# Performance work log

Hardware: AMD Instinct MI355X
Metric: run time of the kernel (lower is better)

## Reference

```python
import jax, jax.numpy as jnp
import numpy as np
from functools import partial

H = 512
V = 32000


def setup_inputs() -> dict:
    key = jax.random.key(0)
    ks = jax.random.split(key, 16)
    B, Td, Te = 16, 64, 64
    s = 0.02
    inp = {
        'input_seqs': jax.random.normal(ks[0], (B, Td, H), jnp.float32),
        'input_lengths': jax.random.randint(ks[1], (B,), 1, Td + 1, jnp.int32),
        'encoder_outputs': jax.random.normal(ks[2], (B, Te, H), jnp.float32),
        'encoder_length': jax.random.randint(ks[3], (B,), 1, Te + 1, jnp.int32),
        # GRU (1 layer, batch_first): PyTorch layout W_ih (3H,H), W_hh (3H,H)
        'W_ih': jax.random.normal(ks[4], (3 * H, H), jnp.float32) * s,
        'W_hh': jax.random.normal(ks[5], (3 * H, H), jnp.float32) * s,
        'b_ih': jnp.zeros((3 * H,), jnp.float32),
        'b_hh': jnp.zeros((3 * H,), jnp.float32),
        # Attn: W: Linear(2H -> H), v: Linear(H -> 1)
        'W_attn': jax.random.normal(ks[6], (H, 2 * H), jnp.float32) * s,
        'b_attn': jnp.zeros((H,), jnp.float32),
        'v_w': jax.random.normal(ks[7], (H,), jnp.float32) * s,
        'v_b': jnp.zeros((), jnp.float32),
        # dense: Linear(2H -> H), output: Linear(H -> V)
        'W_dense': jax.random.normal(ks[8], (H, 2 * H), jnp.float32) * s,
        'b_dense': jnp.zeros((H,), jnp.float32),
        'W_out': jax.random.normal(ks[9], (V, H), jnp.float32) * s,
        'b_out': jnp.zeros((V,), jnp.float32),
    }
    return inp


def gru_forward(x, lengths, W_ih, W_hh, b_ih, b_hh):
    # Emulates pack_padded_sequence + GRU + pad_packed_sequence:
    # hidden state frozen past each sequence's length, outputs zero there.
    B, T, Hd = x.shape
    x_proj = jnp.einsum('bth,gh->btg', x, W_ih) + b_ih  # (B,T,3H)

    def step(h, inp):
        xp, t = inp  # xp: (B,3H)
        hp = h @ W_hh.T + b_hh
        xr, xz, xn = jnp.split(xp, 3, axis=-1)
        hr, hz, hn = jnp.split(hp, 3, axis=-1)
        r = jax.nn.sigmoid(xr + hr)
        z = jax.nn.sigmoid(xz + hz)
        n = jnp.tanh(xn + r * hn)
        h_new = (1.0 - z) * n + z * h
        valid = (t < lengths)[:, None]
        h_keep = jnp.where(valid, h_new, h)
        y = jnp.where(valid, h_new, 0.0)
        return h_keep, y

    h0 = jnp.zeros((B, Hd), x.dtype)
    h_last, ys = jax.lax.scan(step, h0, (x_proj.swapaxes(0, 1), jnp.arange(T)))
    return ys.swapaxes(0, 1), h_last  # (B,T,H), (B,H)


def attn_forward(enc, dec, enc_len, dec_len, W_attn, b_attn, v_w, v_b):
    B, Te, Hd = enc.shape
    Td = dec.shape[1]
    e_mask = (jnp.arange(Te) < enc_len[:, None])  # (B,Te)
    d_mask = (jnp.arange(Td) < dec_len[:, None])  # (B,Td)
    mask = (d_mask[:, :, None] & e_mask[:, None, :]).astype(enc.dtype)  # (B,Td,Te)
    # split W on the concat axis: cat(enc,dec) @ W.T = enc@We.T + dec@Wd.T
    We, Wd = W_attn[:, :Hd], W_attn[:, Hd:]
    enc_p = jnp.einsum('beh,gh->beg', enc, We)  # (B,Te,H)
    dec_p = jnp.einsum('bdh,gh->bdg', dec, Wd)  # (B,Td,H)
    m4 = mask[..., None]
    # masked-then-projected, matching enc_outputs*mask / dec_outputs*mask in torch
    score = jnp.tanh(enc_p[:, None, :, :] * m4 + dec_p[:, :, None, :] * m4 + b_attn)  # (B,Td,Te,H)
    energy = jnp.einsum('bdeh,h->bde', score, v_w) + v_b  # (B,Td,Te)
    a = jax.nn.softmax(energy, axis=2)  # softmax over ALL Te incl. masked (faithful)
    a_m = a * mask
    s = a_m.sum(axis=2)
    s = jnp.where(s == 0, 1.0, s)
    attention = a_m / s[:, :, None]  # (B,Td,Te)
    # attention is already zero where mask==0, so enc*mask == plain enc here
    context = jnp.einsum('bde,beh->bdh', attention, enc)
    return context  # dropout is identity at eval


def reference(input_seqs, input_lengths, encoder_outputs, encoder_length,
              W_ih, W_hh, b_ih, b_hh, W_attn, b_attn, v_w, v_b,
              W_dense, b_dense, W_out, b_out):
    dec_out, h_last = gru_forward(input_seqs, input_lengths, W_ih, W_hh, b_ih, b_hh)
    context = attn_forward(encoder_outputs, dec_out, encoder_length, input_lengths,
                           W_attn, b_attn, v_w, v_b)
    outputs = jnp.concatenate((dec_out, context), axis=2)  # (B,Td,2H)
    dense = jnp.tanh(jnp.einsum('bdg,hg->bdh', outputs, W_dense) + b_dense)
    logits = jnp.einsum('bdh,vh->bdv', dense, W_out) + b_out  # (B,Td,V)
    return logits, h_last[None]  # hidden: (n_layers=1, B, H)
```

## Files before the change

### kernel.cpp

```cpp
#include <hip/hip_runtime.h>
#include <stdint.h>


#define Hdim 512
#define Vdim 32000
#define Bdim 16
#define Tdim 64
#define BT   1024
#define GANG_BLOCKS 16

typedef __attribute__((ext_vector_type(8))) short bf16x8;
typedef __attribute__((ext_vector_type(4))) float f32x4;

static __device__ __forceinline__ unsigned short f2bf(float f) {
    unsigned u = __float_as_uint(f);
    u = u + 0x7FFFu + ((u >> 16) & 1u);
    return (unsigned short)(u >> 16);
}
static __device__ __forceinline__ float bf2f(unsigned short h) {
    return __uint_as_float((unsigned)h << 16);
}


__global__ void zero_kernel(float* p, int n) {
    int i = blockIdx.x * 256 + threadIdx.x;
    if (i < n) p[i] = 0.f;
}

__global__ void f32_to_bf16_kernel(const float* __restrict__ in,
                                   unsigned short* __restrict__ out, int n) {
    int i = (blockIdx.x * 256 + threadIdx.x) * 4;
    int stride = gridDim.x * 256 * 4;
    for (; i < n; i += stride) {
        float4 v = *(const float4*)(in + i);
        unsigned short h[4] = {f2bf(v.x), f2bf(v.y), f2bf(v.z), f2bf(v.w)};
        *(uint2*)(out + i) = *(const uint2*)h;
    }
}

__global__ void split_bf16_kernel(const float* __restrict__ in,
                                  unsigned short* __restrict__ hi,
                                  unsigned short* __restrict__ lo, int n) {
    int i = (blockIdx.x * 256 + threadIdx.x) * 4;
    int stride = gridDim.x * 256 * 4;
    for (; i < n; i += stride) {
        float4 v = *(const float4*)(in + i);
        float f[4] = {v.x, v.y, v.z, v.w};
        unsigned short h[4], l[4];
#pragma unroll
        for (int k = 0; k < 4; ++k) {
            h[k] = f2bf(f[k]);
            l[k] = f2bf(f[k] - bf2f(h[k]));
        }
        *(uint2*)(hi + i) = *(const uint2*)h;
        *(uint2*)(lo + i) = *(const uint2*)l;
    }
}


__global__ __launch_bounds__(256) void gemm_split(
    const unsigned short* __restrict__ Ah, const unsigned short* __restrict__ Al, int lda,
    const unsigned short* __restrict__ Bh, const unsigned short* __restrict__ Bl, int ldb,
    const float* __restrict__ bias,
    float* __restrict__ C, unsigned short* __restrict__ Cb, int ldc,
    int K, int act)
{
    __shared__ unsigned short AsH[128 * 40];
    __shared__ unsigned short AsL[128 * 40];
    __shared__ unsigned short BsH[128 * 40];
    __shared__ unsigned short BsL[128 * 40];
    const int tid = threadIdx.x;
    const int m0 = blockIdx.y * 128, n0 = blockIdx.x * 128;
    const int wave = tid >> 6, lane = tid & 63;
    const int wm = (wave >> 1) * 64, wn = (wave & 1) * 64;
    const int lrow = lane & 15, lk = (lane >> 4) * 8;

    f32x4 acc[4][4];
#pragma unroll
    for (int i = 0; i < 4; ++i)
#pragma unroll
        for (int j = 0; j < 4; ++j) acc[i][j] = (f32x4){0.f, 0.f, 0.f, 0.f};

    for (int k0 = 0; k0 < K; k0 += 32) {
#pragma unroll
        for (int i = 0; i < 2; ++i) {
            int idx = tid + i * 256;
            int rr = idx >> 2, kq = (idx & 3) * 8;
            size_t ao = (size_t)(m0 + rr) * lda + k0 + kq;
            size_t bo = (size_t)(n0 + rr) * ldb + k0 + kq;
            *(uint4*)(&AsH[rr * 40 + kq]) = *(const uint4*)(Ah + ao);
            *(uint4*)(&AsL[rr * 40 + kq]) = *(const uint4*)(Al + ao);
            *(uint4*)(&BsH[rr * 40 + kq]) = *(const uint4*)(Bh + bo);
            *(uint4*)(&BsL[rr * 40 + kq]) = *(const uint4*)(Bl + bo);
        }
        __syncthreads();
        bf16x8 ah[4], al[4], bh[4], bl[4];
#pragma unroll
        for (int i = 0; i < 4; ++i) {
            ah[i] = *(const bf16x8*)(&AsH[(wm + i * 16 + lrow) * 40 + lk]);
            al[i] = *(const bf16x8*)(&AsL[(wm + i * 16 + lrow) * 40 + lk]);
        }
#pragma unroll
        for (int j = 0; j < 4; ++j) {
            bh[j] = *(const bf16x8*)(&BsH[(wn + j * 16 + lrow) * 40 + lk]);
            bl[j] = *(const bf16x8*)(&BsL[(wn + j * 16 + lrow) * 40 + lk]);
        }
#pragma unroll
        for (int i = 0; i < 4; ++i)
#pragma unroll
            for (int j = 0; j < 4; ++j) {
                acc[i][j] = __builtin_amdgcn_mfma_f32_16x16x32_bf16(ah[i], bh[j], acc[i][j], 0, 0, 0);
                acc[i][j] = __builtin_amdgcn_mfma_f32_16x16x32_bf16(ah[i], bl[j], acc[i][j], 0, 0, 0);
                acc[i][j] = __builtin_amdgcn_mfma_f32_16x16x32_bf16(al[i], bh[j], acc[i][j], 0, 0, 0);
            }
        __syncthreads();
    }

    const int crow = m0 + wm + ((lane >> 4) * 4);
    const int ccol = n0 + wn + (lane & 15);
#pragma unroll
    for (int i = 0; i < 4; ++i) {
#pragma unroll
        for (int j = 0; j < 4; ++j) {
            int col = ccol + j * 16;
            float bv = bias[col];
#pragma unroll
            for (int rr = 0; rr < 4; ++rr) {
                int row = crow + i * 16 + rr;
                float v = acc[i][j][rr] + bv;
                if (act == 1) v = tanhf(v);
                if (Cb) Cb[(size_t)row * ldc + col] = f2bf(v);
                else    C [(size_t)row * ldc + col] = v;
            }
        }
    }
}


static __device__ __forceinline__ void agent_st(float* p, float v) {
    __hip_atomic_store(p, v, __ATOMIC_RELAXED, __HIP_MEMORY_SCOPE_AGENT);
}

__global__ __launch_bounds__(512) void gru_persistent(
    const float* __restrict__ xp,
    const float* __restrict__ Whh,
    const float* __restrict__ bhh,
    const int*   __restrict__ lengths,
    float* __restrict__ hbuf,
    int*   __restrict__ sync,
    unsigned short* __restrict__ cath,
    unsigned short* __restrict__ catl,
    float* __restrict__ h_last)
{
    const int bid  = blockIdx.x;
    const int b    = bid >> 4;
    const int blk  = bid & 15;
    const int tid  = threadIdx.x;
    const int wave = tid >> 6, lane = tid & 63;
    const int j0 = blk * 32 + wave * 4;
    const int k0 = lane * 8;

    float w[12][8];
#pragma unroll
    for (int g = 0; g < 3; ++g)
#pragma unroll
        for (int jj = 0; jj < 4; ++jj) {
            const float* src = Whh + (size_t)(g * 512 + j0 + jj) * Hdim + k0;
            float4 a = *(const float4*)src;
            float4 bq = *(const float4*)(src + 4);
            int r = g * 4 + jj;
            w[r][0] = a.x;  w[r][1] = a.y;  w[r][2] = a.z;  w[r][3] = a.w;
            w[r][4] = bq.x; w[r][5] = bq.y; w[r][6] = bq.z; w[r][7] = bq.w;
        }

    const int j = j0 + (lane & 3);
    float bh_r = 0.f, bh_z = 0.f, bh_n = 0.f;
    if (lane < 4) {
        bh_r = bhh[j]; bh_z = bhh[512 + j]; bh_n = bhh[1024 + j];
    }
    const int len_b = lengths[b];
    float hprev = 0.f;

    int* flags = sync + b * 64;
    const float* xbase = xp + (size_t)b * Tdim * 1536;

    for (int t = 0; t < Tdim; ++t) {
        const float* hcur = hbuf + (t & 1) * (Bdim * Hdim) + b * Hdim;
        float*       hnxt = hbuf + ((t + 1) & 1) * (Bdim * Hdim) + b * Hdim;

        float xr = 0.f, xz = 0.f, xn = 0.f;
        if (lane < 4) {
            const float* xrow = xbase + (size_t)t * 1536;
            xr = xrow[j]; xz = xrow[512 + j]; xn = xrow[1024 + j];
        }

        const unsigned long long* hp = (const unsigned long long*)(hcur + k0);
        float hv[8];
#pragma unroll
        for (int q = 0; q < 4; ++q) {
            unsigned long long u =
                __hip_atomic_load(hp + q, __ATOMIC_RELAXED, __HIP_MEMORY_SCOPE_AGENT);
            union { unsigned long long u; float f[2]; } cv; cv.u = u;
            hv[q * 2]     = cv.f[0];
            hv[q * 2 + 1] = cv.f[1];
        }

        float p[12];
#pragma unroll
        for (int r = 0; r < 12; ++r) {
            float s = 0.f;
#pragma unroll
            for (int k = 0; k < 8; ++k) s += w[r][k] * hv[k];
            p[r] = s;
        }

#pragma unroll
        for (int off = 1; off < 64; off <<= 1)
#pragma unroll
            for (int r = 0; r < 12; ++r)
                p[r] += __shfl_xor(p[r], off);

        if (lane < 4) {
            const int jj = lane;
            float hr = p[jj]     + bh_r;
            float hz = p[4 + jj] + bh_z;
            float hn = p[8 + jj] + bh_n;
            float rg = 1.f / (1.f + __expf(-(xr + hr)));
            float zg = 1.f / (1.f + __expf(-(xz + hz)));
            float ng = tanhf(xn + rg * hn);
            float hnew = (1.f - zg) * ng + zg * hprev;
            bool valid = t < len_b;
            float hkeep = valid ? hnew : hprev;
            hprev = hkeep;
            agent_st(hnxt + j, hkeep);
            float y = valid ? hnew : 0.f;
            unsigned short yh = f2bf(y);
            size_t ci = (size_t)(b * Tdim + t) * 1024 + j;
            cath[ci] = yh;
            catl[ci] = f2bf(y - bf2f(yh));
            if (t == Tdim - 1) h_last[b * Hdim + j] = hkeep;
        }

        if (t == Tdim - 1) break;
        __asm__ volatile("" ::: "memory");
        __builtin_amdgcn_s_waitcnt(0);
        __asm__ volatile("" ::: "memory");
        __syncthreads();
        if (wave == 0) {
            if (lane == 0)
                __hip_atomic_store(&flags[blk], t + 1, __ATOMIC_RELAXED,
                                   __HIP_MEMORY_SCOPE_AGENT);
            for (;;) {
                int v = t + 1;
                if (lane < GANG_BLOCKS)
                    v = __hip_atomic_load(&flags[lane], __ATOMIC_RELAXED,
                                          __HIP_MEMORY_SCOPE_AGENT);
                if (__all(v >= t + 1)) break;
                __builtin_amdgcn_s_sleep(1);
            }
        }
        __syncthreads();
        __asm__ volatile("" ::: "memory");
    }
}


__global__ __launch_bounds__(256) void attn_kernel(
    const float* __restrict__ encp,
    const float* __restrict__ decp,
    const float* __restrict__ enc,
    const float* __restrict__ battn,
    const float* __restrict__ vw,
    const float* __restrict__ vb,
    const int* __restrict__ enc_len,
    const int* __restrict__ dec_len,
    unsigned short* __restrict__ cath,
    unsigned short* __restrict__ catl)
{
    const int blk = blockIdx.x;
    const int b = blk >> 6, d = blk & 63;
    const int tid = threadIdx.x;
    const size_t obase = (size_t)(b * Tdim + d) * 1024 + 512;

    if (d >= dec_len[b]) {
        for (int h = tid; h < Hdim; h += 256) { cath[obase + h] = 0; catl[obase + h] = 0; }
        return;
    }
    const int Tv = enc_len[b];

    __shared__ float part[64][4];
    __shared__ float a_lds[64];

    const int e = tid >> 2, p = tid & 3;
    float s = 0.f;
    if (e < Tv) {
        const float* ep = encp + (size_t)(b * Tdim + e) * Hdim;
        const float* dp = decp + (size_t)(b * Tdim + d) * Hdim;
        const int g0 = p * 128;
        for (int g = g0; g < g0 + 128; ++g)
            s += vw[g] * tanhf(ep[g] + dp[g] + battn[g]);
    }
    part[e][p] = s;
    __syncthreads();

    if (tid < 64) {
        const int e2 = tid;
        float en = (e2 < Tv) ? (part[e2][0] + part[e2][1] + part[e2][2] + part[e2][3] + vb[0]) : -1e30f;
        float m = en;
#pragma unroll
        for (int off = 32; off; off >>= 1) m = fmaxf(m, __shfl_xor(m, off));
        float ex = (e2 < Tv) ? __expf(en - m) : 0.f;
        float sum = ex;
#pragma unroll
        for (int off = 32; off; off >>= 1) sum += __shfl_xor(sum, off);
        a_lds[e2] = ex / sum;
    }
    __syncthreads();

    const int h = tid * 2;
    float c0 = 0.f, c1 = 0.f;
    for (int e3 = 0; e3 < Tv; ++e3) {
        float a = a_lds[e3];
        float2 ev = *(const float2*)(enc + (size_t)(b * Tdim + e3) * Hdim + h);
        c0 += a * ev.x; c1 += a * ev.y;
    }
    unsigned short h0 = f2bf(c0), h1 = f2bf(c1);
    cath[obase + h]     = h0;  catl[obase + h]     = f2bf(c0 - bf2f(h0));
    cath[obase + h + 1] = h1;  catl[obase + h + 1] = f2bf(c1 - bf2f(h1));
}


__global__ __launch_bounds__(256) void gemm_logits(
    const unsigned short* __restrict__ A,
    const unsigned short* __restrict__ B,
    const float* __restrict__ bias,
    float* __restrict__ C)
{
    const int K = Hdim;
    __shared__ unsigned short As[128 * 40];
    __shared__ unsigned short Bs[128 * 40];
    const int tid = threadIdx.x;
    const int m0 = blockIdx.y * 128, n0 = blockIdx.x * 128;
    const int wave = tid >> 6, lane = tid & 63;
    const int wm = (wave >> 1) * 64, wn = (wave & 1) * 64;
    const int lrow = lane & 15, lk = (lane >> 4) * 8;

    f32x4 acc[4][4];
#pragma unroll
    for (int i = 0; i < 4; ++i)
#pragma unroll
        for (int j = 0; j < 4; ++j) acc[i][j] = (f32x4){0.f, 0.f, 0.f, 0.f};

    for (int k0 = 0; k0 < K; k0 += 32) {
#pragma unroll
        for (int i = 0; i < 2; ++i) {
            int idx = tid + i * 256;
            int rr = idx >> 2, kq = (idx & 3) * 8;
            *(uint4*)(&As[rr * 40 + kq]) = *(const uint4*)(A + (size_t)(m0 + rr) * K + k0 + kq);
            *(uint4*)(&Bs[rr * 40 + kq]) = *(const uint4*)(B + (size_t)(n0 + rr) * K + k0 + kq);
        }
        __syncthreads();
        bf16x8 af[4], bf[4];
#pragma unroll
        for (int i = 0; i < 4; ++i) af[i] = *(const bf16x8*)(&As[(wm + i * 16 + lrow) * 40 + lk]);
#pragma unroll
        for (int j = 0; j < 4; ++j) bf[j] = *(const bf16x8*)(&Bs[(wn + j * 16 + lrow) * 40 + lk]);
#pragma unroll
        for (int i = 0; i < 4; ++i)
#pragma unroll
            for (int j = 0; j < 4; ++j)
                acc[i][j] = __builtin_amdgcn_mfma_f32_16x16x32_bf16(af[i], bf[j], acc[i][j], 0, 0, 0);
        __syncthreads();
    }

    const int crow = m0 + wm + ((lane >> 4) * 4);
    const int ccol = n0 + wn + (lane & 15);
#pragma unroll
    for (int i = 0; i < 4; ++i) {
#pragma unroll
        for (int j = 0; j < 4; ++j) {
            int col = ccol + j * 16;
            float bv = bias[col];
#pragma unroll
            for (int rr = 0; rr < 4; ++rr) {
                int row = crow + i * 16 + rr;
                C[(size_t)row * Vdim + col] = acc[i][j][rr] + bv;
            }
        }
    }
}


extern "C" void kernel_launch(void* const* d_in, const int* in_sizes, int n_in,
                              void* d_out, int out_size, void* d_ws, size_t ws_size,
                              hipStream_t stream) {
    (void)in_sizes; (void)n_in; (void)out_size; (void)ws_size;

    const float* input_seqs  = (const float*)d_in[0];
    const int*   input_len   = (const int*)  d_in[1];
    const float* enc_out     = (const float*)d_in[2];
    const int*   enc_len     = (const int*)  d_in[3];
    const float* W_ih        = (const float*)d_in[4];
    const float* W_hh        = (const float*)d_in[5];
    const float* b_ih        = (const float*)d_in[6];
    const float* b_hh        = (const float*)d_in[7];
    const float* W_attn      = (const float*)d_in[8];
    const float* b_attn      = (const float*)d_in[9];
    const float* v_w         = (const float*)d_in[10];
    const float* v_b         = (const float*)d_in[11];
    const float* W_dense     = (const float*)d_in[12];
    const float* b_dense     = (const float*)d_in[13];
    const float* W_out       = (const float*)d_in[14];
    const float* b_out       = (const float*)d_in[15];

    float* logits = (float*)d_out;
    float* h_last = (float*)d_out + (size_t)BT * Vdim;

    float* ws    = (float*)d_ws;
    float* xp    = ws;
    float* encp  = xp   + 1572864;
    float* decp  = encp + 524288;
    float* hbuf  = decp + 524288;
    float* zbias = hbuf + 16384;
    int*   sync  = (int*)decp;
    unsigned short* U0 = (unsigned short*)(zbias + 512);
    unsigned short* inp_h   = U0;
    unsigned short* inp_l   = U0 + 524288;
    unsigned short* Wih_h   = U0 + 1048576;
    unsigned short* Wih_l   = U0 + 1835008;
    unsigned short* Wattn_h = U0 + 2621440;
    unsigned short* Wattn_l = U0 + 3145728;
    unsigned short* Wden_h  = U0 + 3670016;
    unsigned short* Wden_l  = U0 + 4194304;
    unsigned short* enc_h   = U0 + 4718592;
    unsigned short* enc_l   = U0 + 5242880;
    unsigned short* Wout_bf = U0 + 5767168;
    unsigned short* cath = U0;
    unsigned short* catl = U0 + 1048576;
    unsigned short* dense_bf = (unsigned short*)encp;

    zero_kernel<<<(16384 + 512 + 255) / 256, 256, 0, stream>>>(hbuf, 16384 + 512);
    zero_kernel<<<4, 256, 0, stream>>>((float*)sync, 1024);
    f32_to_bf16_kernel<<<4096, 256, 0, stream>>>(W_out, Wout_bf, Vdim * Hdim);
    split_bf16_kernel<<<256, 256, 0, stream>>>(input_seqs, inp_h, inp_l, BT * Hdim);
    split_bf16_kernel<<<256, 256, 0, stream>>>(W_ih, Wih_h, Wih_l, 1536 * Hdim);
    split_bf16_kernel<<<256, 256, 0, stream>>>(W_attn, Wattn_h, Wattn_l, Hdim * 1024);
    split_bf16_kernel<<<256, 256, 0, stream>>>(W_dense, Wden_h, Wden_l, Hdim * 1024);
    split_bf16_kernel<<<256, 256, 0, stream>>>(enc_out, enc_h, enc_l, BT * Hdim);

    gemm_split<<<dim3(1536 / 128, BT / 128), 256, 0, stream>>>(
        inp_h, inp_l, Hdim, Wih_h, Wih_l, Hdim, b_ih, xp, nullptr, 1536, Hdim, 0);

    gemm_split<<<dim3(Hdim / 128, BT / 128), 256, 0, stream>>>(
        enc_h, enc_l, Hdim, Wattn_h, Wattn_l, 1024, zbias, encp, nullptr, Hdim, Hdim, 0);

    gru_persistent<<<Bdim * GANG_BLOCKS, 512, 0, stream>>>(
        xp, W_hh, b_hh, input_len, hbuf, sync, cath, catl, h_last);

    gemm_split<<<dim3(Hdim / 128, BT / 128), 256, 0, stream>>>(
        cath, catl, 1024, Wattn_h + 512, Wattn_l + 512, 1024, zbias, decp, nullptr, Hdim, Hdim, 0);

    attn_kernel<<<BT, 256, 0, stream>>>(encp, decp, enc_out, b_attn, v_w, v_b,
                                        enc_len, input_len, cath, catl);

    gemm_split<<<dim3(Hdim / 128, BT / 128), 256, 0, stream>>>(
        cath, catl, 1024, Wden_h, Wden_l, 1024, b_dense, nullptr, dense_bf, Hdim, 1024, 1);

    gemm_logits<<<dim3(Vdim / 128, BT / 128), 256, 0, stream>>>(
        dense_bf, Wout_bf, b_out, logits);
}
```

Measured before the change: 729.1 us.

## Replace GRU barrier with tagged h slots, fuse preprocessing, convert W_out in-GEMM

The GRU persistent kernel drops the per-step flag barrier and global-memory waitcnt. Each hidden value is now stored as a 64-bit word carrying the step index, and consumers spin until every tag matches before staging h in shared memory. The separate zero and split kernels are merged into one preprocessing launch. The standalone W_out bf16 conversion is removed, and the logits GEMM now converts fp32 W_out to bf16 while loading tiles. This trades launch overhead and barrier latency for fp32 weight reads in the logits GEMM, converted redundantly by each M-tile block.

```diff
diff --git a/kernel.cpp b/kernel.cpp
--- a/kernel.cpp
+++ b/kernel.cpp
@@ -22,29 +22,51 @@
 }
 
 
-__global__ void zero_kernel(float* p, int n) {
-    int i = blockIdx.x * 256 + threadIdx.x;
-    if (i < n) p[i] = 0.f;
-}
-
-__global__ void f32_to_bf16_kernel(const float* __restrict__ in,
-                                   unsigned short* __restrict__ out, int n) {
-    int i = (blockIdx.x * 256 + threadIdx.x) * 4;
-    int stride = gridDim.x * 256 * 4;
-    for (; i < n; i += stride) {
-        float4 v = *(const float4*)(in + i);
-        unsigned short h[4] = {f2bf(v.x), f2bf(v.y), f2bf(v.z), f2bf(v.w)};
-        *(uint2*)(out + i) = *(const uint2*)h;
-    }
-}
-
-__global__ void split_bf16_kernel(const float* __restrict__ in,
-                                  unsigned short* __restrict__ hi,
-                                  unsigned short* __restrict__ lo, int n) {
-    int i = (blockIdx.x * 256 + threadIdx.x) * 4;
-    int stride = gridDim.x * 256 * 4;
-    for (; i < n; i += stride) {
-        float4 v = *(const float4*)(in + i);
+#define U_ZERO 8320
+#define U_INP  131072
+#define U_WIH  196608
+#define U_WAT  131072
+#define U_WDE  131072
+#define U_ENC  131072
+#define U_TOT  (U_ZERO + U_INP + U_WIH + U_WAT + U_WDE + U_ENC)
+
+__global__ __launch_bounds__(256) void preproc_kernel(
+    const float* __restrict__ input_seqs,
+    const float* __restrict__ W_ih,
+    const float* __restrict__ W_attn,
+    const float* __restrict__ W_dense,
+    const float* __restrict__ enc,
+    float* __restrict__ zero_base,
+    unsigned short* __restrict__ inp_h, unsigned short* __restrict__ inp_l,
+    unsigned short* __restrict__ Wih_h, unsigned short* __restrict__ Wih_l,
+    unsigned short* __restrict__ Wat_h, unsigned short* __restrict__ Wat_l,
+    unsigned short* __restrict__ Wde_h, unsigned short* __restrict__ Wde_l,
+    unsigned short* __restrict__ enc_h, unsigned short* __restrict__ enc_l)
+{
+    int u = blockIdx.x * 256 + threadIdx.x;
+    const int stride = gridDim.x * 256;
+    for (; u < U_TOT; u += stride) {
+        int r = u;
+        if (r < U_ZERO) {
+            float4 z; z.x = 0.f; z.y = 0.f; z.z = 0.f; z.w = 0.f;
+            *(float4*)(zero_base + r * 4) = z;
+            continue;
+        }
+        r -= U_ZERO;
+        const float* src; unsigned short* hi; unsigned short* lo;
+        if (r < U_INP) { src = input_seqs; hi = inp_h; lo = inp_l; }
+        else { r -= U_INP;
+            if (r < U_WIH) { src = W_ih; hi = Wih_h; lo = Wih_l; }
+            else { r -= U_WIH;
+                if (r < U_WAT) { src = W_attn; hi = Wat_h; lo = Wat_l; }
+                else { r -= U_WAT;
+                    if (r < U_WDE) { src = W_dense; hi = Wde_h; lo = Wde_l; }
+                    else { r -= U_WDE; src = enc; hi = enc_h; lo = enc_l; }
+                }
+            }
+        }
+        int i = r * 4;
+        float4 v = *(const float4*)(src + i);
         float f[4] = {v.x, v.y, v.z, v.w};
         unsigned short h[4], l[4];
 #pragma unroll
@@ -137,17 +159,12 @@
 }
 
 
-static __device__ __forceinline__ void agent_st(float* p, float v) {
-    __hip_atomic_store(p, v, __ATOMIC_RELAXED, __HIP_MEMORY_SCOPE_AGENT);
-}
-
 __global__ __launch_bounds__(512) void gru_persistent(
     const float* __restrict__ xp,
     const float* __restrict__ Whh,
     const float* __restrict__ bhh,
     const int*   __restrict__ lengths,
-    float* __restrict__ hbuf,
-    int*   __restrict__ sync,
+    unsigned long long* __restrict__ hslots,
     unsigned short* __restrict__ cath,
     unsigned short* __restrict__ catl,
     float* __restrict__ h_last)
@@ -160,6 +177,8 @@
     const int j0 = blk * 32 + wave * 4;
     const int k0 = lane * 8;
 
+    __shared__ float hl[2][512];
+
     float w[12][8];
 #pragma unroll
     for (int g = 0; g < 3; ++g)
@@ -181,12 +200,12 @@
     const int len_b = lengths[b];
     float hprev = 0.f;
 
-    int* flags = sync + b * 64;
+    const size_t PSTR = (size_t)Bdim * Hdim;
+    unsigned long long* gslot = hslots + (size_t)b * Hdim;
     const float* xbase = xp + (size_t)b * Tdim * 1536;
 
     for (int t = 0; t < Tdim; ++t) {
-        const float* hcur = hbuf + (t & 1) * (Bdim * Hdim) + b * Hdim;
-        float*       hnxt = hbuf + ((t + 1) & 1) * (Bdim * Hdim) + b * Hdim;
+        const int par = t & 1;
 
         float xr = 0.f, xz = 0.f, xn = 0.f;
         if (lane < 4) {
@@ -194,16 +213,29 @@
             xr = xrow[j]; xz = xrow[512 + j]; xn = xrow[1024 + j];
         }
 
-        const unsigned long long* hp = (const unsigned long long*)(hcur + k0);
+        if (wave == 0) {
+            const unsigned long long* sl = gslot + (size_t)par * PSTR + k0;
+            unsigned long long v[8];
+            bool ok;
+            do {
+#pragma unroll
+                for (int q = 0; q < 8; ++q)
+                    v[q] = __hip_atomic_load(sl + q, __ATOMIC_RELAXED,
+                                             __HIP_MEMORY_SCOPE_AGENT);
+                ok = true;
+#pragma unroll
+                for (int q = 0; q < 8; ++q)
+                    ok = ok && ((unsigned)(v[q] >> 32) == (unsigned)t);
+            } while (!ok);
+#pragma unroll
+            for (int q = 0; q < 8; ++q)
+                hl[par][k0 + q] = __uint_as_float((unsigned)v[q]);
+        }
+        __syncthreads();
+
         float hv[8];
 #pragma unroll
-        for (int q = 0; q < 4; ++q) {
-            unsigned long long u =
-                __hip_atomic_load(hp + q, __ATOMIC_RELAXED, __HIP_MEMORY_SCOPE_AGENT);
-            union { unsigned long long u; float f[2]; } cv; cv.u = u;
-            hv[q * 2]     = cv.f[0];
-            hv[q * 2 + 1] = cv.f[1];
-        }
+        for (int q = 0; q < 8; ++q) hv[q] = hl[par][k0 + q];
 
         float p[12];
 #pragma unroll
@@ -232,35 +264,21 @@
             bool valid = t < len_b;
             float hkeep = valid ? hnew : hprev;
             hprev = hkeep;
-            agent_st(hnxt + j, hkeep);
+            if (t < Tdim - 1) {
+                unsigned long long pv =
+                    ((unsigned long long)(unsigned)(t + 1) << 32) |
+                    (unsigned long long)__float_as_uint(hkeep);
+                __hip_atomic_store(gslot + (size_t)((t + 1) & 1) * PSTR + j, pv,
+                                   __ATOMIC_RELAXED, __HIP_MEMORY_SCOPE_AGENT);
+            } else {
+                h_last[b * Hdim + j] = hkeep;
+            }
             float y = valid ? hnew : 0.f;
             unsigned short yh = f2bf(y);
             size_t ci = (size_t)(b * Tdim + t) * 1024 + j;
             cath[ci] = yh;
             catl[ci] = f2bf(y - bf2f(yh));
-            if (t == Tdim - 1) h_last[b * Hdim + j] = hkeep;
-        }
-
-        if (t == Tdim - 1) break;
-        __asm__ volatile("" ::: "memory");
-        __builtin_amdgcn_s_waitcnt(0);
-        __asm__ volatile("" ::: "memory");
-        __syncthreads();
-        if (wave == 0) {
-            if (lane == 0)
-                __hip_atomic_store(&flags[blk], t + 1, __ATOMIC_RELAXED,
-                                   __HIP_MEMORY_SCOPE_AGENT);
-            for (;;) {
-                int v = t + 1;
-                if (lane < GANG_BLOCKS)
-                    v = __hip_atomic_load(&flags[lane], __ATOMIC_RELAXED,
-                                          __HIP_MEMORY_SCOPE_AGENT);
-                if (__all(v >= t + 1)) break;
-                __builtin_amdgcn_s_sleep(1);
-            }
-        }
-        __syncthreads();
-        __asm__ volatile("" ::: "memory");
+        }
     }
 }
 
@@ -332,7 +350,7 @@
 
 __global__ __launch_bounds__(256) void gemm_logits(
     const unsigned short* __restrict__ A,
-    const unsigned short* __restrict__ B,
+    const float* __restrict__ Bf,
     const float* __restrict__ bias,
     float* __restrict__ C)
 {
@@ -357,7 +375,12 @@
             int idx = tid + i * 256;
             int rr = idx >> 2, kq = (idx & 3) * 8;
             *(uint4*)(&As[rr * 40 + kq]) = *(const uint4*)(A + (size_t)(m0 + rr) * K + k0 + kq);
-            *(uint4*)(&Bs[rr * 40 + kq]) = *(const uint4*)(B + (size_t)(n0 + rr) * K + k0 + kq);
+            const float* bp = Bf + (size_t)(n0 + rr) * K + k0 + kq;
+            float4 b0 = *(const float4*)bp;
+            float4 b1 = *(const float4*)(bp + 4);
+            unsigned short hb[8] = {f2bf(b0.x), f2bf(b0.y), f2bf(b0.z), f2bf(b0.w),
+                                    f2bf(b1.x), f2bf(b1.y), f2bf(b1.z), f2bf(b1.w)};
+            *(uint4*)(&Bs[rr * 40 + kq]) = *(const uint4*)hb;
         }
         __syncthreads();
         bf16x8 af[4], bf[4];
@@ -420,9 +443,8 @@
     float* xp    = ws;
     float* encp  = xp   + 1572864;
     float* decp  = encp + 524288;
-    float* hbuf  = decp + 524288;
-    float* zbias = hbuf + 16384;
-    int*   sync  = (int*)decp;
+    unsigned long long* hslots = (unsigned long long*)(decp + 524288);
+    float* zbias = (float*)(hslots + 16384);
     unsigned short* U0 = (unsigned short*)(zbias + 512);
     unsigned short* inp_h   = U0;
     unsigned short* inp_l   = U0 + 524288;
@@ -434,19 +456,15 @@
     unsigned short* Wden_l  = U0 + 4194304;
     unsigned short* enc_h   = U0 + 4718592;
     unsigned short* enc_l   = U0 + 5242880;
-    unsigned short* Wout_bf = U0 + 5767168;
     unsigned short* cath = U0;
     unsigned short* catl = U0 + 1048576;
     unsigned short* dense_bf = (unsigned short*)encp;
 
-    zero_kernel<<<(16384 + 512 + 255) / 256, 256, 0, stream>>>(hbuf, 16384 + 512);
-    zero_kernel<<<4, 256, 0, stream>>>((float*)sync, 1024);
-    f32_to_bf16_kernel<<<4096, 256, 0, stream>>>(W_out, Wout_bf, Vdim * Hdim);
-    split_bf16_kernel<<<256, 256, 0, stream>>>(input_seqs, inp_h, inp_l, BT * Hdim);
-    split_bf16_kernel<<<256, 256, 0, stream>>>(W_ih, Wih_h, Wih_l, 1536 * Hdim);
-    split_bf16_kernel<<<256, 256, 0, stream>>>(W_attn, Wattn_h, Wattn_l, Hdim * 1024);
-    split_bf16_kernel<<<256, 256, 0, stream>>>(W_dense, Wden_h, Wden_l, Hdim * 1024);
-    split_bf16_kernel<<<256, 256, 0, stream>>>(enc_out, enc_h, enc_l, BT * Hdim);
+    preproc_kernel<<<2849, 256, 0, stream>>>(
+        input_seqs, W_ih, W_attn, W_dense, enc_out,
+        (float*)hslots,
+        inp_h, inp_l, Wih_h, Wih_l, Wattn_h, Wattn_l,
+        Wden_h, Wden_l, enc_h, enc_l);
 
     gemm_split<<<dim3(1536 / 128, BT / 128), 256, 0, stream>>>(
         inp_h, inp_l, Hdim, Wih_h, Wih_l, Hdim, b_ih, xp, nullptr, 1536, Hdim, 0);
@@ -455,7 +473,7 @@
         enc_h, enc_l, Hdim, Wattn_h, Wattn_l, 1024, zbias, encp, nullptr, Hdim, Hdim, 0);
 
     gru_persistent<<<Bdim * GANG_BLOCKS, 512, 0, stream>>>(
-        xp, W_hh, b_hh, input_len, hbuf, sync, cath, catl, h_last);
+        xp, W_hh, b_hh, input_len, hslots, cath, catl, h_last);
 
     gemm_split<<<dim3(Hdim / 128, BT / 128), 256, 0, stream>>>(
         cath, catl, 1024, Wattn_h + 512, Wattn_l + 512, 1024, zbias, decp, nullptr, Hdim, Hdim, 0);
@@ -467,5 +485,5 @@
         cath, catl, 1024, Wden_h, Wden_l, 1024, b_dense, nullptr, dense_bf, Hdim, 1024, 1);
 
     gemm_logits<<<dim3(Vdim / 128, BT / 128), 256, 0, stream>>>(
-        dense_bf, Wout_bf, b_out, logits);
-}
+        dense_bf, W_out, b_out, logits);
+}
```

After: 709.8 us. -2.6%, faster.
